# Kernel tuning notes

Hardware: AMD Instinct MI355X
Metric: run time of the kernel (lower is better)

The kernel has to match this reference:

```python
import jax, jax.numpy as jnp
import numpy as np

B, SEG, MEM, D, E, H = 4, 1024, 1024, 128, 128, 8  # model_dim == embed_dim required by module
TOTAL = SEG + MEM


def sinusoid_pos(length, e):
    # Transformer-XL relative sinusoid table, then flipped so row 0 = largest distance
    p = jnp.arange(length, dtype=jnp.float32)[:, None]
    j = jnp.arange(e, dtype=jnp.float32)[None, :]
    ang = p / jnp.power(jnp.float32(10000.0), 2.0 * j / e)
    enc = jnp.where((jnp.arange(e) % 2 == 0)[None, :], jnp.sin(ang), jnp.cos(ang))
    return enc[::-1]


def circulant_shift(b, shift):
    # b: (B, H, S, W). Row i of the index matrix is the rolled arange shifted by (shift - i).
    W = b.shape[-1]
    S = b.shape[-2]
    idx = jnp.roll(jnp.arange(W), shift)[::-1]
    idx2 = jnp.concatenate([idx, idx])
    win = idx2[jnp.arange(S)[:, None] + jnp.arange(W)[None, :]][:, ::-1]  # (S, W)
    return jnp.take_along_axis(b, win[None, None, :, :], axis=3)


def setup_inputs() -> dict:
    key = jax.random.key(0)
    ks = jax.random.split(key, 11)
    w = 0.02  # small init for linear weights (Linear default-ish scale)
    return {
        "x": jax.random.normal(ks[0], (B, SEG, D), dtype=jnp.float32),
        "mem": jax.random.normal(ks[1], (B, MEM, D), dtype=jnp.float32),
        "att_mask": jnp.zeros((SEG, TOTAL), dtype=bool),  # unused by the module's forward
        "u1": jax.random.normal(ks[2], (H, 1, E), dtype=jnp.float32),
        "u2": jax.random.normal(ks[3], (H, 1, E), dtype=jnp.float32),
        "w_q": jax.random.normal(ks[4], (D, H * E), dtype=jnp.float32) * w,
        "w_kv": jax.random.normal(ks[5], (D, 2 * H * E), dtype=jnp.float32) * w,
        "w_r": jax.random.normal(ks[6], (D, H * E), dtype=jnp.float32) * w,
        "w_mlp": jax.random.normal(ks[7], (H * E, D), dtype=jnp.float32) * w,
        "ln_g": jnp.ones((D,), dtype=jnp.float32),
        "ln_b": jnp.zeros((D,), dtype=jnp.float32),
    }


def reference(x, mem, att_mask, u1, u2, w_q, w_kv, w_r, w_mlp, ln_g, ln_b):
    bsz, seg, d = x.shape
    h = jnp.concatenate((mem, x), axis=1)          # (B, total, D)
    total = h.shape[1]
    mem_len = total - seg

    # NB: the original uses .view without transpose -> plain row-major reshape
    q = (x @ w_q).reshape(bsz, -1, seg, d)          # (B, H, S, E)
    kv = (h @ w_kv).reshape(2 * bsz, -1, total, d)  # (2B, H, T, E)
    k, v = kv[:bsz], kv[bsz:]

    pos = sinusoid_pos(total, d)                    # buffer pos[-total:]
    r = (pos @ w_r).reshape(-1, total, d)           # (H, T, E)

    b = jnp.einsum('bhse,hte->bhst', q, r)
    b = circulant_shift(b, -seg + 1)

    qk = jnp.einsum('bhse,bhte->bhst', q, k)
    u1k = jnp.einsum('he,bhte->bht', u1[:, 0], k)[:, :, None, :]
    u2r = jnp.einsum('he,hte->ht', u2[:, 0], r)[None, :, None, :]

    score = qk + b + u1k + u2r                      # (B, H, S, T)
    tri = (jnp.arange(total)[None, :] - jnp.arange(seg)[:, None]) <= mem_len
    score = jnp.where(tri[None, None], score, 0.0) / jnp.sqrt(jnp.float32(d))
    score = jnp.where(score == 0.0, -jnp.inf, score)  # faithful zeros->-inf trick
    score = jax.nn.softmax(score, axis=-1)

    att = jnp.einsum('bhst,bhte->bhse', score, v).reshape(bsz, seg, -1)
    y = att @ w_mlp + x
    mu = jnp.mean(y, axis=-1, keepdims=True)
    var = jnp.mean((y - mu) ** 2, axis=-1, keepdims=True)
    return (y - mu) / jnp.sqrt(var + 1e-5) * ln_g + ln_b
```

## Files before the change

### kernel.cpp

```cpp
#include <hip/hip_runtime.h>
#include <hip/hip_bf16.h>
#include <stdint.h>

typedef __bf16 bf16;
typedef __attribute__((ext_vector_type(8))) __bf16 bf16x8;
typedef __attribute__((ext_vector_type(4))) __bf16 bf16x4;
typedef __attribute__((ext_vector_type(4))) float f32x4;

#define KSC 0.12764932952880681f

__device__ __forceinline__ f32x4 MFMA(bf16x8 a, bf16x8 b, f32x4 c) {
  return __builtin_amdgcn_mfma_f32_16x16x32_bf16(a, b, c, 0, 0, 0);
}

__device__ __forceinline__ void GLL16(const void* g, void* l) {
  __builtin_amdgcn_global_load_lds(
      (const __attribute__((address_space(1))) void*)g,
      (__attribute__((address_space(3))) void*)l, 16, 0, 0);
}

__device__ __forceinline__ bf16 tobf(float f) { return (bf16)f; }

__global__ __launch_bounds__(256) void k_prep(
    const float* __restrict__ x, const float* __restrict__ mm,
    const float* __restrict__ wq, const float* __restrict__ wkv,
    const float* __restrict__ wr, const float* __restrict__ wmlp,
    bf16* __restrict__ posb, bf16* __restrict__ wq_bt, bf16* __restrict__ wkv_bt,
    bf16* __restrict__ wr_bt, bf16* __restrict__ wmlp_bt,
    bf16* __restrict__ xb, bf16* __restrict__ memb)
{
  int id = blockIdx.x * 256 + threadIdx.x;
  if (id < 262144) {
    int t = id >> 7, j = id & 127;
    float p = (float)(2047 - t);
    float ang = p * exp2f(-(float)j * 0.20762050593046264f);
    float v = ((j & 1) == 0) ? sinf(ang) : cosf(ang);
    posb[id] = tobf(v);
    return;
  }
  id -= 262144;
  if (id < 131072) { int k = id >> 10, n = id & 1023; wq_bt[n * 128 + k] = tobf(wq[id]); return; }
  id -= 131072;
  if (id < 262144) { int k = id >> 11, n = id & 2047; wkv_bt[n * 128 + k] = tobf(wkv[id]); return; }
  id -= 262144;
  if (id < 131072) { int k = id >> 10, n = id & 1023; wr_bt[n * 128 + k] = tobf(wr[id]); return; }
  id -= 131072;
  if (id < 131072) { int k = id >> 7, n = id & 127; wmlp_bt[n * 1024 + k] = tobf(wmlp[id]); return; }
  id -= 131072;
  if (id < 131072) {
    f32x4 v = *(const f32x4*)(x + (size_t)id * 4);
    bf16x4 o; o[0]=tobf(v[0]); o[1]=tobf(v[1]); o[2]=tobf(v[2]); o[3]=tobf(v[3]);
    *(bf16x4*)(xb + (size_t)id * 4) = o;
    return;
  }
  id -= 131072;
  if (id < 131072) {
    f32x4 v = *(const f32x4*)(mm + (size_t)id * 4);
    bf16x4 o; o[0]=tobf(v[0]); o[1]=tobf(v[1]); o[2]=tobf(v[2]); o[3]=tobf(v[3]);
    *(bf16x4*)(memb + (size_t)id * 4) = o;
  }
}

template <int MODE>
__global__ __launch_bounds__(256, 2) void k_proj(
    const bf16* __restrict__ asrc, const bf16* __restrict__ asrc2,
    const bf16* __restrict__ wbt, bf16* __restrict__ out0, bf16* __restrict__ out1,
    const float* __restrict__ u1, const float* __restrict__ u2)
{
  __shared__ bf16 As[64 * 128];
  __shared__ bf16 Bs[128 * 128];
  const int m0 = blockIdx.x * 64;
  const int n0 = blockIdx.y * 128;
  const int tid = threadIdx.x;
  const int w = tid >> 6, lane = tid & 63, g = lane >> 4, c = lane & 15;

#pragma unroll
  for (int it = 0; it < 4; ++it) {
    int ch = w * 256 + it * 64 + lane;
    int row = ch >> 4, cc = ch & 15;
    int scc = cc ^ (row & 7);
    const bf16* src;
    if (MODE == 1) {
      int rg = m0 + row;
      int bb = rg >> 11, t = rg & 2047;
      src = (t < 1024) ? (asrc2 + (size_t)(bb * 1024 + t) * 128)
                       : (asrc + (size_t)(bb * 1024 + (t - 1024)) * 128);
    } else {
      src = asrc + (size_t)(m0 + row) * 128;
    }
    GLL16(src + scc * 8, (char*)As + (w * 256 + it * 64) * 16);
  }
#pragma unroll
  for (int it = 0; it < 8; ++it) {
    int ch = w * 512 + it * 64 + lane;
    int n = ch >> 4, cc = ch & 15;
    int scc = cc ^ (n & 7);
    GLL16(wbt + (size_t)(n0 + n) * 128 + scc * 8, (char*)Bs + (w * 512 + it * 64) * 16);
  }
  __syncthreads();

  f32x4 acc[8] = {};
#pragma unroll
  for (int kk = 0; kk < 4; ++kk) {
    bf16x8 a = *(const bf16x8*)((const char*)As + (16 * w + c) * 256 + (((4 * kk + g) ^ (c & 7)) << 4));
#pragma unroll
    for (int fo = 0; fo < 8; ++fo) {
      bf16x8 b = *(const bf16x8*)((const char*)Bs + (16 * fo + c) * 256 + (((4 * kk + g) ^ (c & 7)) << 4));
      acc[fo] = MFMA(a, b, acc[fo]);
    }
  }

#pragma unroll
  for (int fo = 0; fo < 8; ++fo) {
#pragma unroll
    for (int j = 0; j < 4; ++j) {
      int rg = m0 + 16 * w + 4 * g + j;
      int cg = n0 + 16 * fo + c;
      float av = acc[fo][j];
      if (MODE == 0) {
        int b = rg >> 10, s2 = rg & 1023;
        int nn = s2 >> 7;
        int s = ((s2 & 127) << 3) | (cg >> 7);
        int e = cg & 127;
        size_t idx = ((size_t)((b * 8 + nn) * 1024 + s)) * 128 + e;
        out0[idx] = tobf((av + u1[nn * 128 + e]) * KSC);
        out1[idx] = tobf((av + u2[nn * 128 + e]) * KSC);
      } else if (MODE == 1) {
        int bb = rg >> 11, t = rg & 2047;
        int nn = (t >> 7) & 7;
        int hlf = (t >> 10) & 1;
        int t2 = ((t & 127) << 4) | (cg >> 7);
        int e = cg & 127;
        bf16 v = tobf(av);
        if (bb < 2)
          out0[((size_t)(((2 * bb + hlf) * 8 + nn) * 2048 + t2)) * 128 + e] = v;
        else
          out1[((size_t)(((2 * (bb - 2) + hlf) * 8 + nn) * 2048 + t2)) * 128 + e] = v;
      } else {
        int nn = rg >> 8;
        int t = ((rg & 255) << 3) | (cg >> 7);
        int e = cg & 127;
        bf16 v = tobf(av);
        out0[((size_t)(nn * 2112 + t)) * 128 + e] = v;
        if (t < 64) out0[((size_t)(nn * 2112 + 2048 + t)) * 128 + e] = v;
      }
    }
  }
}

__global__ __launch_bounds__(256) void k_vtrans(const bf16* __restrict__ vh, bf16* __restrict__ vht)
{
  __shared__ bf16 T[64][72];
  int bt = blockIdx.x * 64, be = blockIdx.y * 64, bh = blockIdx.z;
  const bf16* src = vh + (size_t)bh * 2048 * 128;
  bf16* dst = vht + (size_t)bh * 128 * 2048;
#pragma unroll
  for (int i2 = 0; i2 < 2; ++i2) {
    int ch = i2 * 256 + threadIdx.x;
    int tt = ch >> 3, cc = ch & 7;
    bf16x8 v = *(const bf16x8*)(src + (size_t)(bt + tt) * 128 + be + cc * 8);
    *(bf16x8*)&T[tt][cc * 8] = v;
  }
  __syncthreads();
#pragma unroll
  for (int i2 = 0; i2 < 2; ++i2) {
    int ch = i2 * 256 + threadIdx.x;
    int ee = ch >> 3, c2 = ch & 7;
    bf16x8 o;
#pragma unroll
    for (int m = 0; m < 8; ++m) o[m] = T[c2 * 8 + m][ee];
    *(bf16x8*)(dst + (size_t)(be + ee) * 2048 + bt + c2 * 8) = o;
  }
}

__global__ __launch_bounds__(256, 2) void k_flash(
    const bf16* __restrict__ qhk, const bf16* __restrict__ qhr,
    const bf16* __restrict__ kh, const bf16* __restrict__ vht,
    const bf16* __restrict__ rhe, bf16* __restrict__ att2)
{
  __shared__ bf16 Ks[2][64 * 128];
  __shared__ bf16 Vs[2][64 * 128];
  __shared__ char QRS[4][2688];

  const int x = blockIdx.x;
  const int bh = x & 31;
  const int qb = (x < 256) ? (x >> 5) : (15 - ((x - 256) >> 5));
  const int ib = bh >> 3, nh = bh & 7;
  const int s0 = qb * 64;
  const int tid = threadIdx.x;
  const int w = tid >> 6, lane = tid & 63, g = lane >> 4, c = lane & 15;

  const bf16* qkb  = qhk + (size_t)bh * 1024 * 128;
  const bf16* qrb  = qhr + (size_t)bh * 1024 * 128;
  const bf16* kbase = kh + (size_t)bh * 2048 * 128;
  const bf16* vbase = vht + (size_t)bh * 128 * 2048;
  const bf16* rbase = rhe + (size_t)nh * 2112 * 128;

  const int nt = qb + 17;

  const bf16 *kp0, *kp1, *vp0, *vp1, *vp2, *vp3;
  {
    int ch0 = w * 256 + lane;
    int ch1 = ch0 + 64;
    int r0 = ch0 >> 4, cc0 = ch0 & 15;
    int r1 = ch1 >> 4, cc1 = ch1 & 15;
    kp0 = kbase + (size_t)r0 * 128 + (cc0 ^ (r0 & 7)) * 8;
    kp1 = kbase + (size_t)r1 * 128 + (cc1 ^ (r1 & 7)) * 8;
    int e0 = ch0 >> 3, t0c = ch0 & 7;
    int e1 = ch1 >> 3, t1c = ch1 & 7;
    int e2 = e0 + 16, e3 = e1 + 16;
    vp0 = vbase + (size_t)e0 * 2048 + (t0c ^ (e0 & 7)) * 8;
    vp1 = vbase + (size_t)e1 * 2048 + (t1c ^ (e1 & 7)) * 8;
    vp2 = vbase + (size_t)e2 * 2048 + (t0c ^ (e2 & 7)) * 8;
    vp3 = vbase + (size_t)e3 * 2048 + (t1c ^ (e3 & 7)) * 8;
  }
  const int dof = (w * 256 + lane) * 16;

  auto stage = [&](char* Kd, char* Vd) {
    GLL16(kp0, Kd + dof);
    GLL16(kp1, Kd + dof + 1024);
    GLL16(kp0 + 1024, Kd + dof + 2048);
    GLL16(kp1 + 1024, Kd + dof + 3072);
    GLL16(vp0, Vd + dof);
    GLL16(vp1, Vd + dof + 1024);
    GLL16(vp2, Vd + dof + 2048);
    GLL16(vp3, Vd + dof + 3072);
    kp0 += 8192; kp1 += 8192;
    vp0 += 64; vp1 += 64; vp2 += 64; vp3 += 64;
  };

  bf16x8 qfK[4], qfR[4];
  {
    int srow = s0 + 16 * w + c;
#pragma unroll
    for (int kk = 0; kk < 4; ++kk) {
      qfK[kk] = *(const bf16x8*)(qkb + (size_t)srow * 128 + kk * 32 + g * 8);
      qfR[kk] = *(const bf16x8*)(qrb + (size_t)srow * 128 + kk * 32 + g * 8);
    }
  }

  bf16x8 rf[5][4];
  const bf16* rp[5];
  {
    const int L0 = 1008 - s0 - 16 * w + c;
#pragma unroll
    for (int f2 = 0; f2 < 5; ++f2) {
      rp[f2] = rbase + (size_t)(L0 + 16 * f2) * 128 + g * 8;
#pragma unroll
      for (int kk = 0; kk < 4; ++kk) rf[f2][kk] = *(const bf16x8*)(rp[f2] + kk * 32);
      rp[f2] += 64 * 128;
    }
  }

  f32x4 Ot[8] = {};
  float m_r = -1e30f, l_r = 0.f;

  stage((char*)Ks[0], (char*)Vs[0]);

  for (int tt = 0; tt < nt; ++tt) {
    __syncthreads();
    const bool notlast = (tt + 1 < nt);
    if (notlast) stage((char*)Ks[(tt + 1) & 1], (char*)Vs[(tt + 1) & 1]);

    const bf16* Kc = Ks[tt & 1];
    const bf16* Vc = Vs[tt & 1];

    f32x4 sacc[4] = {};
    __builtin_amdgcn_s_setprio(1);
#pragma unroll
    for (int kk = 0; kk < 4; ++kk) {
#pragma unroll
      for (int f = 0; f < 4; ++f) {
        bf16x8 kf = *(const bf16x8*)((const char*)Kc + (16 * f + c) * 256 + (((4 * kk + g) ^ (c & 7)) << 4));
        sacc[f] = MFMA(kf, qfK[kk], sacc[f]);
      }
    }
    f32x4 bacc[5] = {};
#pragma unroll
    for (int f2 = 0; f2 < 5; ++f2)
#pragma unroll
      for (int kk = 0; kk < 4; ++kk)
        bacc[f2] = MFMA(rf[f2][kk], qfR[kk], bacc[f2]);
    __builtin_amdgcn_s_setprio(0);

    bf16* qrw = (bf16*)QRS[w];
#pragma unroll
    for (int f2 = 0; f2 < 5; ++f2)
#pragma unroll
      for (int j = 0; j < 4; ++j)
        qrw[c * 82 + 16 * f2 + 4 * g + j] = tobf(bacc[f2][j]);

    if (notlast) {
#pragma unroll
      for (int f2 = 0; f2 < 5; ++f2) {
#pragma unroll
        for (int kk = 0; kk < 4; ++kk) rf[f2][kk] = *(const bf16x8*)(rp[f2] + kk * 32);
        rp[f2] += 64 * 128;
      }
    }

    float zv[4][4];
#pragma unroll
    for (int f = 0; f < 4; ++f)
#pragma unroll
      for (int j = 0; j < 4; ++j) {
        int tl = 16 * f + 4 * g + j;
        float z = sacc[f][j] + (float)qrw[c * 82 + (tl - c + 15)];
        if (!notlast && (tl > 16 * w + c)) z = -1e30f;
        zv[f][j] = z;
      }

    float pm = fmaxf(fmaxf(fmaxf(zv[0][0], zv[0][1]), fmaxf(zv[0][2], zv[0][3])),
                     fmaxf(fmaxf(zv[1][0], zv[1][1]), fmaxf(zv[1][2], zv[1][3])));
    float pm2 = fmaxf(fmaxf(fmaxf(zv[2][0], zv[2][1]), fmaxf(zv[2][2], zv[2][3])),
                      fmaxf(fmaxf(zv[3][0], zv[3][1]), fmaxf(zv[3][2], zv[3][3])));
    pm = fmaxf(pm, pm2);
    pm = fmaxf(pm, __shfl_xor(pm, 16));
    pm = fmaxf(pm, __shfl_xor(pm, 32));

    float alpha = 1.f;
    if (!__all(pm <= m_r + 8.0f)) {
      float mn = fmaxf(m_r, pm);
      alpha = exp2f(m_r - mn);
      m_r = mn;
      float at[4];
#pragma unroll
      for (int j = 0; j < 4; ++j) at[j] = __shfl(alpha, 20 * g + j);
#pragma unroll
      for (int fo = 0; fo < 8; ++fo)
#pragma unroll
        for (int j = 0; j < 4; ++j) Ot[fo][j] *= at[j];
    }

    float ps = 0.f;
#pragma unroll
    for (int f = 0; f < 4; ++f)
#pragma unroll
      for (int j = 0; j < 4; ++j) { float pp = exp2f(zv[f][j] - m_r); zv[f][j] = pp; ps += pp; }
    ps += __shfl_xor(ps, 16);
    ps += __shfl_xor(ps, 32);
    l_r = l_r * alpha + ps;

    bf16* pw = (bf16*)QRS[w];
#pragma unroll
    for (int f = 0; f < 4; ++f)
#pragma unroll
      for (int j = 0; j < 4; ++j) {
        int t = 16 * f + 4 * g + j;
        pw[c * 80 + ((((t >> 3) ^ (c & 7)) << 3) | (t & 7))] = tobf(zv[f][j]);
      }

    __builtin_amdgcn_s_setprio(1);
#pragma unroll
    for (int kk2 = 0; kk2 < 2; ++kk2) {
      bf16x8 pa = *(const bf16x8*)(pw + c * 80 + (((4 * kk2 + g) ^ (c & 7)) << 3));
#pragma unroll
      for (int fo = 0; fo < 8; ++fo) {
        int e = 16 * fo + c;
        bf16x8 vf = *(const bf16x8*)((const char*)Vc + e * 128 + (((4 * kk2 + g) ^ (c & 7)) << 4));
        Ot[fo] = MFMA(pa, vf, Ot[fo]);
      }
    }
    __builtin_amdgcn_s_setprio(0);
  }

  float linv[4];
#pragma unroll
  for (int j = 0; j < 4; ++j) linv[j] = 1.f / __shfl(l_r, 20 * g + j);
  bf16* ob = att2 + (size_t)ib * 1024 * 1024;
#pragma unroll
  for (int j = 0; j < 4; ++j) {
    int sg = s0 + 16 * w + 4 * g + j;
    size_t rowb = (size_t)(nh * 128 + (sg >> 3)) * 1024 + ((sg & 7) << 7);
#pragma unroll
    for (int fo = 0; fo < 8; ++fo)
      ob[rowb + 16 * fo + c] = tobf(Ot[fo][j] * linv[j]);
  }
}

__global__ __launch_bounds__(256, 2) void k_mlp(
    const bf16* __restrict__ att2, const bf16* __restrict__ wmlp_bt,
    const float* __restrict__ x, const float* __restrict__ lng, const float* __restrict__ lnb,
    float* __restrict__ out)
{
  __shared__ bf16 As[64 * 128];
  __shared__ bf16 Bs[128 * 128];
  const int m0 = blockIdx.x * 64;
  const int tid = threadIdx.x;
  const int w = tid >> 6, lane = tid & 63, g = lane >> 4, c = lane & 15;

  f32x4 acc[8] = {};
  for (int ks = 0; ks < 8; ++ks) {
    int k0 = ks * 128;
    __syncthreads();
#pragma unroll
    for (int it = 0; it < 4; ++it) {
      int ch = w * 256 + it * 64 + lane;
      int row = ch >> 4, cc = ch & 15;
      GLL16(att2 + (size_t)(m0 + row) * 1024 + k0 + ((cc ^ (row & 7)) * 8),
            (char*)As + (w * 256 + it * 64) * 16);
    }
#pragma unroll
    for (int it = 0; it < 8; ++it) {
      int ch = w * 512 + it * 64 + lane;
      int n = ch >> 4, cc = ch & 15;
      GLL16(wmlp_bt + (size_t)n * 1024 + k0 + ((cc ^ (n & 7)) * 8),
            (char*)Bs + (w * 512 + it * 64) * 16);
    }
    __syncthreads();
#pragma unroll
    for (int kk = 0; kk < 4; ++kk) {
      bf16x8 a = *(const bf16x8*)((const char*)As + (16 * w + c) * 256 + (((4 * kk + g) ^ (c & 7)) << 4));
#pragma unroll
      for (int fo = 0; fo < 8; ++fo) {
        bf16x8 b = *(const bf16x8*)((const char*)Bs + (16 * fo + c) * 256 + (((4 * kk + g) ^ (c & 7)) << 4));
        acc[fo] = MFMA(a, b, acc[fo]);
      }
    }
  }
#pragma unroll
  for (int j = 0; j < 4; ++j) {
    int rg = m0 + 16 * w + 4 * g + j;
    float y[8];
    float s1 = 0.f, s2 = 0.f;
#pragma unroll
    for (int fo = 0; fo < 8; ++fo) {
      float v = acc[fo][j] + x[(size_t)rg * 128 + 16 * fo + c];
      y[fo] = v; s1 += v; s2 += v * v;
    }
#pragma unroll
    for (int d = 1; d < 16; d <<= 1) { s1 += __shfl_xor(s1, d); s2 += __shfl_xor(s2, d); }
    float mu = s1 * 0.0078125f;
    float var = s2 * 0.0078125f - mu * mu;
    float rs = rsqrtf(var + 1e-5f);
#pragma unroll
    for (int fo = 0; fo < 8; ++fo) {
      int e = 16 * fo + c;
      out[(size_t)rg * 128 + e] = (y[fo] - mu) * rs * lng[e] + lnb[e];
    }
  }
}

extern "C" void kernel_launch(void* const* d_in, const int* in_sizes, int n_in,
                              void* d_out, int out_size, void* d_ws, size_t ws_size,
                              hipStream_t stream)
{
  const float* x    = (const float*)d_in[0];
  const float* mm   = (const float*)d_in[1];
  const float* u1   = (const float*)d_in[3];
  const float* u2   = (const float*)d_in[4];
  const float* wq   = (const float*)d_in[5];
  const float* wkv  = (const float*)d_in[6];
  const float* wr   = (const float*)d_in[7];
  const float* wmlp = (const float*)d_in[8];
  const float* lng  = (const float*)d_in[9];
  const float* lnb  = (const float*)d_in[10];
  float* out = (float*)d_out;

  char* p = (char*)d_ws;
  bf16* posb    = (bf16*)p;  p += (size_t)262144 * 2;
  bf16* wq_bt   = (bf16*)p;  p += (size_t)131072 * 2;
  bf16* wkv_bt  = (bf16*)p;  p += (size_t)262144 * 2;
  bf16* wr_bt   = (bf16*)p;  p += (size_t)131072 * 2;
  bf16* wmlp_bt = (bf16*)p;  p += (size_t)131072 * 2;
  bf16* xb      = (bf16*)p;  p += (size_t)524288 * 2;
  bf16* memb    = (bf16*)p;  p += (size_t)524288 * 2;
  bf16* qhk     = (bf16*)p;  p += (size_t)4 * 8 * 1024 * 128 * 2;
  bf16* qhr     = (bf16*)p;  p += (size_t)4 * 8 * 1024 * 128 * 2;
  bf16* kh      = (bf16*)p;  p += (size_t)4 * 8 * 2048 * 128 * 2;
  bf16* vh      = (bf16*)p;  p += (size_t)4 * 8 * 2048 * 128 * 2;
  bf16* vht     = (bf16*)p;  p += (size_t)4 * 8 * 2048 * 128 * 2;
  bf16* rhe     = (bf16*)p;  p += (size_t)8 * 2112 * 128 * 2;
  bf16* att2    = (bf16*)p;  p += (size_t)4 * 1024 * 1024 * 2;

  k_prep<<<dim3(4608), dim3(256), 0, stream>>>(x, mm, wq, wkv, wr, wmlp,
                                               posb, wq_bt, wkv_bt, wr_bt, wmlp_bt, xb, memb);
  k_proj<0><<<dim3(64, 8),   dim3(256), 0, stream>>>(xb,  (const bf16*)nullptr, wq_bt,  qhk, qhr, u1, u2);
  k_proj<1><<<dim3(128, 16), dim3(256), 0, stream>>>(xb,  memb,                 wkv_bt, kh,  vh,  nullptr, nullptr);
  k_proj<2><<<dim3(32, 8),   dim3(256), 0, stream>>>(posb,(const bf16*)nullptr, wr_bt,  rhe, (bf16*)nullptr, nullptr, nullptr);
  k_vtrans<<<dim3(32, 2, 32), dim3(256), 0, stream>>>(vh, vht);
  k_flash<<<dim3(512), dim3(256), 0, stream>>>(qhk, qhr, kh, vht, rhe, att2);
  k_mlp<<<dim3(64), dim3(256), 0, stream>>>(att2, wmlp_bt, x, lng, lnb, out);
}
```

Before: 273.9 us.

## Split flash attention over KV halves with combine kernel, single-buffer LDS

Splits each query block's key range into two halves processed by separate workgroups (1024 blocks instead of 512), writing fp16 partial outputs plus running max and sum, which a new combine kernel merges into att2. LDS drops to single-buffered K/V with staged loads interleaved around an extra barrier, allowing three blocks per CU. The prep kernel now transposes weights through shared-memory tiles for coalesced access and uses fast sin/cos intrinsics. This adds a combine pass and extra global traffic for the partials, and reduces load/compute overlap inside each block.

```diff
diff --git a/kernel.cpp b/kernel.cpp
--- a/kernel.cpp
+++ b/kernel.cpp
@@ -3,8 +3,10 @@
 #include <stdint.h>
 
 typedef __bf16 bf16;
+typedef _Float16 f16;
 typedef __attribute__((ext_vector_type(8))) __bf16 bf16x8;
 typedef __attribute__((ext_vector_type(4))) __bf16 bf16x4;
+typedef __attribute__((ext_vector_type(8))) _Float16 f16x8;
 typedef __attribute__((ext_vector_type(4))) float f32x4;
 
 #define KSC 0.12764932952880681f
@@ -29,35 +31,48 @@
     bf16* __restrict__ wr_bt, bf16* __restrict__ wmlp_bt,
     bf16* __restrict__ xb, bf16* __restrict__ memb)
 {
-  int id = blockIdx.x * 256 + threadIdx.x;
-  if (id < 262144) {
+  __shared__ float T[32][33];
+  const int b = blockIdx.x;
+  const int tid = threadIdx.x;
+  if (b < 1024) {
+    int id = b * 256 + tid;
     int t = id >> 7, j = id & 127;
     float p = (float)(2047 - t);
     float ang = p * exp2f(-(float)j * 0.20762050593046264f);
-    float v = ((j & 1) == 0) ? sinf(ang) : cosf(ang);
+    float v = ((j & 1) == 0) ? __sinf(ang) : __cosf(ang);
     posb[id] = tobf(v);
     return;
   }
-  id -= 262144;
-  if (id < 131072) { int k = id >> 10, n = id & 1023; wq_bt[n * 128 + k] = tobf(wq[id]); return; }
-  id -= 131072;
-  if (id < 262144) { int k = id >> 11, n = id & 2047; wkv_bt[n * 128 + k] = tobf(wkv[id]); return; }
-  id -= 262144;
-  if (id < 131072) { int k = id >> 10, n = id & 1023; wr_bt[n * 128 + k] = tobf(wr[id]); return; }
-  id -= 131072;
-  if (id < 131072) { int k = id >> 7, n = id & 127; wmlp_bt[n * 1024 + k] = tobf(wmlp[id]); return; }
-  id -= 131072;
-  if (id < 131072) {
-    f32x4 v = *(const f32x4*)(x + (size_t)id * 4);
-    bf16x4 o; o[0]=tobf(v[0]); o[1]=tobf(v[1]); o[2]=tobf(v[2]); o[3]=tobf(v[3]);
-    *(bf16x4*)(xb + (size_t)id * 4) = o;
+  if (b < 1664) {
+    int tb = b - 1024;
+    const float* src; bf16* dst; int R, C, r0, c0;
+    if (tb < 128)      { src = wq;   dst = wq_bt;   R = 128;  C = 1024; r0 = (tb >> 5) * 32;        c0 = (tb & 31) * 32; }
+    else if (tb < 384) { int t2 = tb - 128; src = wkv;  dst = wkv_bt;  R = 128;  C = 2048; r0 = (t2 >> 6) * 32; c0 = (t2 & 63) * 32; }
+    else if (tb < 512) { int t2 = tb - 384; src = wr;   dst = wr_bt;   R = 128;  C = 1024; r0 = (t2 >> 5) * 32; c0 = (t2 & 31) * 32; }
+    else               { int t2 = tb - 512; src = wmlp; dst = wmlp_bt; R = 1024; C = 128;  r0 = (t2 >> 2) * 32; c0 = (t2 & 3) * 32; }
+    int r = tid >> 3, c4 = (tid & 7) * 4;
+    f32x4 v = *(const f32x4*)(src + (size_t)(r0 + r) * C + c0 + c4);
+    T[r][c4] = v[0]; T[r][c4 + 1] = v[1]; T[r][c4 + 2] = v[2]; T[r][c4 + 3] = v[3];
+    __syncthreads();
+    bf16x4 o;
+#pragma unroll
+    for (int k = 0; k < 4; ++k) o[k] = tobf(T[c4 + k][r]);
+    *(bf16x4*)(dst + (size_t)(c0 + r) * R + r0 + c4) = o;
     return;
   }
-  id -= 131072;
-  if (id < 131072) {
-    f32x4 v = *(const f32x4*)(mm + (size_t)id * 4);
-    bf16x4 o; o[0]=tobf(v[0]); o[1]=tobf(v[1]); o[2]=tobf(v[2]); o[3]=tobf(v[3]);
-    *(bf16x4*)(memb + (size_t)id * 4) = o;
+  {
+    int cb = b - 1664;
+    if (cb < 512) {
+      int i = cb * 256 + tid;
+      f32x4 v = *(const f32x4*)(x + (size_t)i * 4);
+      bf16x4 o; o[0]=tobf(v[0]); o[1]=tobf(v[1]); o[2]=tobf(v[2]); o[3]=tobf(v[3]);
+      *(bf16x4*)(xb + (size_t)i * 4) = o;
+    } else {
+      int i = (cb - 512) * 256 + tid;
+      f32x4 v = *(const f32x4*)(mm + (size_t)i * 4);
+      bf16x4 o; o[0]=tobf(v[0]); o[1]=tobf(v[1]); o[2]=tobf(v[2]); o[3]=tobf(v[3]);
+      *(bf16x4*)(memb + (size_t)i * 4) = o;
+    }
   }
 }
 
@@ -173,30 +188,36 @@
   }
 }
 
-__global__ __launch_bounds__(256, 2) void k_flash(
+__global__ __launch_bounds__(256, 3) void k_flash(
     const bf16* __restrict__ qhk, const bf16* __restrict__ qhr,
     const bf16* __restrict__ kh, const bf16* __restrict__ vht,
-    const bf16* __restrict__ rhe, bf16* __restrict__ att2)
-{
-  __shared__ bf16 Ks[2][64 * 128];
-  __shared__ bf16 Vs[2][64 * 128];
+    const bf16* __restrict__ rhe,
+    f16* __restrict__ part_O, float* __restrict__ part_m, float* __restrict__ part_l)
+{
+  __shared__ bf16 Ks[64 * 128];
+  __shared__ bf16 Vs[64 * 128];
   __shared__ char QRS[4][2688];
 
   const int x = blockIdx.x;
-  const int bh = x & 31;
-  const int qb = (x < 256) ? (x >> 5) : (15 - ((x - 256) >> 5));
-  const int ib = bh >> 3, nh = bh & 7;
+  const int bh = x >> 5;
+  const int qb = (x >> 1) & 15;
+  const int half = x & 1;
+  const int pidx = x;
+  const int nh = bh & 7;
   const int s0 = qb * 64;
   const int tid = threadIdx.x;
   const int w = tid >> 6, lane = tid & 63, g = lane >> 4, c = lane & 15;
+
+  const int nt = qb + 17;
+  const int h = nt >> 1;
+  const int T0 = half ? h : 0;
+  const int Tend = half ? nt : h;
 
   const bf16* qkb  = qhk + (size_t)bh * 1024 * 128;
   const bf16* qrb  = qhr + (size_t)bh * 1024 * 128;
   const bf16* kbase = kh + (size_t)bh * 2048 * 128;
   const bf16* vbase = vht + (size_t)bh * 128 * 2048;
   const bf16* rbase = rhe + (size_t)nh * 2112 * 128;
-
-  const int nt = qb + 17;
 
   const bf16 *kp0, *kp1, *vp0, *vp1, *vp2, *vp3;
   {
@@ -204,28 +225,34 @@
     int ch1 = ch0 + 64;
     int r0 = ch0 >> 4, cc0 = ch0 & 15;
     int r1 = ch1 >> 4, cc1 = ch1 & 15;
-    kp0 = kbase + (size_t)r0 * 128 + (cc0 ^ (r0 & 7)) * 8;
-    kp1 = kbase + (size_t)r1 * 128 + (cc1 ^ (r1 & 7)) * 8;
+    size_t koff = (size_t)T0 * 64 * 128;
+    kp0 = kbase + koff + (size_t)r0 * 128 + (cc0 ^ (r0 & 7)) * 8;
+    kp1 = kbase + koff + (size_t)r1 * 128 + (cc1 ^ (r1 & 7)) * 8;
     int e0 = ch0 >> 3, t0c = ch0 & 7;
     int e1 = ch1 >> 3, t1c = ch1 & 7;
     int e2 = e0 + 16, e3 = e1 + 16;
-    vp0 = vbase + (size_t)e0 * 2048 + (t0c ^ (e0 & 7)) * 8;
-    vp1 = vbase + (size_t)e1 * 2048 + (t1c ^ (e1 & 7)) * 8;
-    vp2 = vbase + (size_t)e2 * 2048 + (t0c ^ (e2 & 7)) * 8;
-    vp3 = vbase + (size_t)e3 * 2048 + (t1c ^ (e3 & 7)) * 8;
+    int voff = T0 * 64;
+    vp0 = vbase + (size_t)e0 * 2048 + voff + (t0c ^ (e0 & 7)) * 8;
+    vp1 = vbase + (size_t)e1 * 2048 + voff + (t1c ^ (e1 & 7)) * 8;
+    vp2 = vbase + (size_t)e2 * 2048 + voff + (t0c ^ (e2 & 7)) * 8;
+    vp3 = vbase + (size_t)e3 * 2048 + voff + (t1c ^ (e3 & 7)) * 8;
   }
   const int dof = (w * 256 + lane) * 16;
 
-  auto stage = [&](char* Kd, char* Vd) {
+  auto stageK = [&]() {
+    char* Kd = (char*)Ks;
     GLL16(kp0, Kd + dof);
     GLL16(kp1, Kd + dof + 1024);
     GLL16(kp0 + 1024, Kd + dof + 2048);
     GLL16(kp1 + 1024, Kd + dof + 3072);
+    kp0 += 8192; kp1 += 8192;
+  };
+  auto stageV = [&]() {
+    char* Vd = (char*)Vs;
     GLL16(vp0, Vd + dof);
     GLL16(vp1, Vd + dof + 1024);
     GLL16(vp2, Vd + dof + 2048);
     GLL16(vp3, Vd + dof + 3072);
-    kp0 += 8192; kp1 += 8192;
     vp0 += 64; vp1 += 64; vp2 += 64; vp3 += 64;
   };
 
@@ -242,7 +269,7 @@
   bf16x8 rf[5][4];
   const bf16* rp[5];
   {
-    const int L0 = 1008 - s0 - 16 * w + c;
+    const int L0 = 1008 - s0 - 16 * w + c + 64 * T0;
 #pragma unroll
     for (int f2 = 0; f2 < 5; ++f2) {
       rp[f2] = rbase + (size_t)(L0 + 16 * f2) * 128 + g * 8;
@@ -255,15 +282,11 @@
   f32x4 Ot[8] = {};
   float m_r = -1e30f, l_r = 0.f;
 
-  stage((char*)Ks[0], (char*)Vs[0]);
-
-  for (int tt = 0; tt < nt; ++tt) {
+  stageK();
+
+  for (int tt = T0; tt < Tend; ++tt) {
     __syncthreads();
-    const bool notlast = (tt + 1 < nt);
-    if (notlast) stage((char*)Ks[(tt + 1) & 1], (char*)Vs[(tt + 1) & 1]);
-
-    const bf16* Kc = Ks[tt & 1];
-    const bf16* Vc = Vs[tt & 1];
+    stageV();
 
     f32x4 sacc[4] = {};
     __builtin_amdgcn_s_setprio(1);
@@ -271,7 +294,7 @@
     for (int kk = 0; kk < 4; ++kk) {
 #pragma unroll
       for (int f = 0; f < 4; ++f) {
-        bf16x8 kf = *(const bf16x8*)((const char*)Kc + (16 * f + c) * 256 + (((4 * kk + g) ^ (c & 7)) << 4));
+        bf16x8 kf = *(const bf16x8*)((const char*)Ks + (16 * f + c) * 256 + (((4 * kk + g) ^ (c & 7)) << 4));
         sacc[f] = MFMA(kf, qfK[kk], sacc[f]);
       }
     }
@@ -290,15 +313,7 @@
       for (int j = 0; j < 4; ++j)
         qrw[c * 82 + 16 * f2 + 4 * g + j] = tobf(bacc[f2][j]);
 
-    if (notlast) {
-#pragma unroll
-      for (int f2 = 0; f2 < 5; ++f2) {
-#pragma unroll
-        for (int kk = 0; kk < 4; ++kk) rf[f2][kk] = *(const bf16x8*)(rp[f2] + kk * 32);
-        rp[f2] += 64 * 128;
-      }
-    }
-
+    const bool lastT = (tt == nt - 1);
     float zv[4][4];
 #pragma unroll
     for (int f = 0; f < 4; ++f)
@@ -306,7 +321,7 @@
       for (int j = 0; j < 4; ++j) {
         int tl = 16 * f + 4 * g + j;
         float z = sacc[f][j] + (float)qrw[c * 82 + (tl - c + 15)];
-        if (!notlast && (tl > 16 * w + c)) z = -1e30f;
+        if (lastT && (tl > 16 * w + c)) z = -1e30f;
         zv[f][j] = z;
       }
 
@@ -350,6 +365,18 @@
         pw[c * 80 + ((((t >> 3) ^ (c & 7)) << 3) | (t & 7))] = tobf(zv[f][j]);
       }
 
+    __syncthreads();
+    const bool more = (tt + 1 < Tend);
+    if (more) stageK();
+    if (more) {
+#pragma unroll
+      for (int f2 = 0; f2 < 5; ++f2) {
+#pragma unroll
+        for (int kk = 0; kk < 4; ++kk) rf[f2][kk] = *(const bf16x8*)(rp[f2] + kk * 32);
+        rp[f2] += 64 * 128;
+      }
+    }
+
     __builtin_amdgcn_s_setprio(1);
 #pragma unroll
     for (int kk2 = 0; kk2 < 2; ++kk2) {
@@ -357,24 +384,59 @@
 #pragma unroll
       for (int fo = 0; fo < 8; ++fo) {
         int e = 16 * fo + c;
-        bf16x8 vf = *(const bf16x8*)((const char*)Vc + e * 128 + (((4 * kk2 + g) ^ (c & 7)) << 4));
+        bf16x8 vf = *(const bf16x8*)((const char*)Vs + e * 128 + (((4 * kk2 + g) ^ (c & 7)) << 4));
         Ot[fo] = MFMA(pa, vf, Ot[fo]);
       }
     }
     __builtin_amdgcn_s_setprio(0);
   }
 
+  if (g == 0) {
+    part_m[pidx * 64 + 16 * w + c] = m_r;
+    part_l[pidx * 64 + 16 * w + c] = l_r;
+  }
   float linv[4];
 #pragma unroll
   for (int j = 0; j < 4; ++j) linv[j] = 1.f / __shfl(l_r, 20 * g + j);
-  bf16* ob = att2 + (size_t)ib * 1024 * 1024;
+  f16* po = part_O + (size_t)pidx * 8192;
 #pragma unroll
   for (int j = 0; j < 4; ++j) {
-    int sg = s0 + 16 * w + 4 * g + j;
-    size_t rowb = (size_t)(nh * 128 + (sg >> 3)) * 1024 + ((sg & 7) << 7);
+    int sl = 16 * w + 4 * g + j;
 #pragma unroll
     for (int fo = 0; fo < 8; ++fo)
-      ob[rowb + 16 * fo + c] = tobf(Ot[fo][j] * linv[j]);
+      po[sl * 128 + 16 * fo + c] = (f16)(Ot[fo][j] * linv[j]);
+  }
+}
+
+__global__ __launch_bounds__(256) void k_combine(
+    const f16* __restrict__ part_O, const float* __restrict__ part_m,
+    const float* __restrict__ part_l, bf16* __restrict__ att2)
+{
+  int ss = blockIdx.x;
+  int bh = ss >> 4, qb = ss & 15;
+  int p1 = (bh << 5) | (qb << 1), p2 = p1 | 1;
+  int r = threadIdx.x >> 2;
+  int e0 = (threadIdx.x & 3) * 32;
+  float m1 = part_m[p1 * 64 + r], m2 = part_m[p2 * 64 + r];
+  float l1 = part_l[p1 * 64 + r], l2 = part_l[p2 * 64 + r];
+  float m = fmaxf(m1, m2);
+  float a1 = exp2f(m1 - m) * l1, a2 = exp2f(m2 - m) * l2;
+  float inv = 1.f / (a1 + a2);
+  a1 *= inv; a2 *= inv;
+  int sg = qb * 64 + r;
+  int ib = bh >> 3, nh = bh & 7;
+  bf16* ob = att2 + (size_t)ib * 1024 * 1024
+           + ((size_t)(nh * 128 + (sg >> 3))) * 1024 + ((sg & 7) << 7);
+  const f16* o1 = part_O + ((size_t)p1 * 64 + r) * 128 + e0;
+  const f16* o2 = part_O + ((size_t)p2 * 64 + r) * 128 + e0;
+#pragma unroll
+  for (int i = 0; i < 32; i += 8) {
+    f16x8 v1 = *(const f16x8*)(o1 + i);
+    f16x8 v2 = *(const f16x8*)(o2 + i);
+    bf16x8 o;
+#pragma unroll
+    for (int k = 0; k < 8; ++k) o[k] = tobf(a1 * (float)v1[k] + a2 * (float)v2[k]);
+    *(bf16x8*)(ob + e0 + i) = o;
   }
 }
 
@@ -473,12 +535,17 @@
   bf16* rhe     = (bf16*)p;  p += (size_t)8 * 2112 * 128 * 2;
   bf16* att2    = (bf16*)p;  p += (size_t)4 * 1024 * 1024 * 2;
 
-  k_prep<<<dim3(4608), dim3(256), 0, stream>>>(x, mm, wq, wkv, wr, wmlp,
+  f16*   part_O = (f16*)vh;
+  float* part_m = (float*)posb;
+  float* part_l = (float*)posb + 65536;
+
+  k_prep<<<dim3(2688), dim3(256), 0, stream>>>(x, mm, wq, wkv, wr, wmlp,
                                                posb, wq_bt, wkv_bt, wr_bt, wmlp_bt, xb, memb);
   k_proj<0><<<dim3(64, 8),   dim3(256), 0, stream>>>(xb,  (const bf16*)nullptr, wq_bt,  qhk, qhr, u1, u2);
   k_proj<1><<<dim3(128, 16), dim3(256), 0, stream>>>(xb,  memb,                 wkv_bt, kh,  vh,  nullptr, nullptr);
   k_proj<2><<<dim3(32, 8),   dim3(256), 0, stream>>>(posb,(const bf16*)nullptr, wr_bt,  rhe, (bf16*)nullptr, nullptr, nullptr);
   k_vtrans<<<dim3(32, 2, 32), dim3(256), 0, stream>>>(vh, vht);
-  k_flash<<<dim3(512), dim3(256), 0, stream>>>(qhk, qhr, kh, vht, rhe, att2);
+  k_flash<<<dim3(1024), dim3(256), 0, stream>>>(qhk, qhr, kh, vht, rhe, part_O, part_m, part_l);
+  k_combine<<<dim3(512), dim3(256), 0, stream>>>(part_O, part_m, part_l, att2);
   k_mlp<<<dim3(64), dim3(256), 0, stream>>>(att2, wmlp_bt, x, lng, lnb, out);
 }
```

Result: slower. 568.7 us (+107.6%).

## Tile weight transposes through LDS, use fast sincos, remap flash blocks per XCD

Applied to the files above, without the earlier changes.

The weight transposes in k_prep now go through a 32x33 shared-memory tile, so both the global reads and the writes are coalesced and vectorised. The old version did scattered scalar stores. The positional sinusoid uses the __sinf/__cosf intrinsics, which can lose accuracy at large angles before bf16 rounding. The flash kernel block index is remapped so that blocks for the same batch-head land on the same XCD (x&7), improving K/V/R reuse in L2 while keeping the long/short q-block balancing. These are several independent changes across two kernels.

```diff
diff --git a/kernel.cpp b/kernel.cpp
--- a/kernel.cpp
+++ b/kernel.cpp
@@ -29,35 +29,48 @@
     bf16* __restrict__ wr_bt, bf16* __restrict__ wmlp_bt,
     bf16* __restrict__ xb, bf16* __restrict__ memb)
 {
-  int id = blockIdx.x * 256 + threadIdx.x;
-  if (id < 262144) {
+  __shared__ float T[32][33];
+  const int b = blockIdx.x;
+  const int tid = threadIdx.x;
+  if (b < 1024) {
+    int id = b * 256 + tid;
     int t = id >> 7, j = id & 127;
     float p = (float)(2047 - t);
     float ang = p * exp2f(-(float)j * 0.20762050593046264f);
-    float v = ((j & 1) == 0) ? sinf(ang) : cosf(ang);
+    float v = ((j & 1) == 0) ? __sinf(ang) : __cosf(ang);
     posb[id] = tobf(v);
     return;
   }
-  id -= 262144;
-  if (id < 131072) { int k = id >> 10, n = id & 1023; wq_bt[n * 128 + k] = tobf(wq[id]); return; }
-  id -= 131072;
-  if (id < 262144) { int k = id >> 11, n = id & 2047; wkv_bt[n * 128 + k] = tobf(wkv[id]); return; }
-  id -= 262144;
-  if (id < 131072) { int k = id >> 10, n = id & 1023; wr_bt[n * 128 + k] = tobf(wr[id]); return; }
-  id -= 131072;
-  if (id < 131072) { int k = id >> 7, n = id & 127; wmlp_bt[n * 1024 + k] = tobf(wmlp[id]); return; }
-  id -= 131072;
-  if (id < 131072) {
-    f32x4 v = *(const f32x4*)(x + (size_t)id * 4);
-    bf16x4 o; o[0]=tobf(v[0]); o[1]=tobf(v[1]); o[2]=tobf(v[2]); o[3]=tobf(v[3]);
-    *(bf16x4*)(xb + (size_t)id * 4) = o;
+  if (b < 1664) {
+    int tb = b - 1024;
+    const float* src; bf16* dst; int R, C, r0, c0;
+    if (tb < 128)      { src = wq;   dst = wq_bt;   R = 128;  C = 1024; r0 = (tb >> 5) * 32;        c0 = (tb & 31) * 32; }
+    else if (tb < 384) { int t2 = tb - 128; src = wkv;  dst = wkv_bt;  R = 128;  C = 2048; r0 = (t2 >> 6) * 32; c0 = (t2 & 63) * 32; }
+    else if (tb < 512) { int t2 = tb - 384; src = wr;   dst = wr_bt;   R = 128;  C = 1024; r0 = (t2 >> 5) * 32; c0 = (t2 & 31) * 32; }
+    else               { int t2 = tb - 512; src = wmlp; dst = wmlp_bt; R = 1024; C = 128;  r0 = (t2 >> 2) * 32; c0 = (t2 & 3) * 32; }
+    int r = tid >> 3, c4 = (tid & 7) * 4;
+    f32x4 v = *(const f32x4*)(src + (size_t)(r0 + r) * C + c0 + c4);
+    T[r][c4] = v[0]; T[r][c4 + 1] = v[1]; T[r][c4 + 2] = v[2]; T[r][c4 + 3] = v[3];
+    __syncthreads();
+    bf16x4 o;
+#pragma unroll
+    for (int k = 0; k < 4; ++k) o[k] = tobf(T[c4 + k][r]);
+    *(bf16x4*)(dst + (size_t)(c0 + r) * R + r0 + c4) = o;
     return;
   }
-  id -= 131072;
-  if (id < 131072) {
-    f32x4 v = *(const f32x4*)(mm + (size_t)id * 4);
-    bf16x4 o; o[0]=tobf(v[0]); o[1]=tobf(v[1]); o[2]=tobf(v[2]); o[3]=tobf(v[3]);
-    *(bf16x4*)(memb + (size_t)id * 4) = o;
+  {
+    int cb = b - 1664;
+    if (cb < 512) {
+      int i = cb * 256 + tid;
+      f32x4 v = *(const f32x4*)(x + (size_t)i * 4);
+      bf16x4 o; o[0]=tobf(v[0]); o[1]=tobf(v[1]); o[2]=tobf(v[2]); o[3]=tobf(v[3]);
+      *(bf16x4*)(xb + (size_t)i * 4) = o;
+    } else {
+      int i = (cb - 512) * 256 + tid;
+      f32x4 v = *(const f32x4*)(mm + (size_t)i * 4);
+      bf16x4 o; o[0]=tobf(v[0]); o[1]=tobf(v[1]); o[2]=tobf(v[2]); o[3]=tobf(v[3]);
+      *(bf16x4*)(memb + (size_t)i * 4) = o;
+    }
   }
 }
 
@@ -183,8 +196,10 @@
   __shared__ char QRS[4][2688];
 
   const int x = blockIdx.x;
-  const int bh = x & 31;
-  const int qb = (x < 256) ? (x >> 5) : (15 - ((x - 256) >> 5));
+  const int xcd = x & 7;
+  const int k2 = x >> 3;
+  const int bh = 8 * (k2 & 3) + xcd;
+  const int qb = (k2 < 32) ? (k2 >> 2) : (23 - (k2 >> 2));
   const int ib = bh >> 3, nh = bh & 7;
   const int s0 = qb * 64;
   const int tid = threadIdx.x;
@@ -216,7 +231,9 @@
   }
   const int dof = (w * 256 + lane) * 16;
 
-  auto stage = [&](char* Kd, char* Vd) {
+  auto stage = [&](int pb) {
+    char* Kd = (char*)Ks[pb];
+    char* Vd = (char*)Vs[pb];
     GLL16(kp0, Kd + dof);
     GLL16(kp1, Kd + dof + 1024);
     GLL16(kp0 + 1024, Kd + dof + 2048);
@@ -255,12 +272,12 @@
   f32x4 Ot[8] = {};
   float m_r = -1e30f, l_r = 0.f;
 
-  stage((char*)Ks[0], (char*)Vs[0]);
+  stage(0);
 
   for (int tt = 0; tt < nt; ++tt) {
     __syncthreads();
     const bool notlast = (tt + 1 < nt);
-    if (notlast) stage((char*)Ks[(tt + 1) & 1], (char*)Vs[(tt + 1) & 1]);
+    if (notlast) stage((tt + 1) & 1);
 
     const bf16* Kc = Ks[tt & 1];
     const bf16* Vc = Vs[tt & 1];
@@ -473,7 +490,7 @@
   bf16* rhe     = (bf16*)p;  p += (size_t)8 * 2112 * 128 * 2;
   bf16* att2    = (bf16*)p;  p += (size_t)4 * 1024 * 1024 * 2;
 
-  k_prep<<<dim3(4608), dim3(256), 0, stream>>>(x, mm, wq, wkv, wr, wmlp,
+  k_prep<<<dim3(2688), dim3(256), 0, stream>>>(x, mm, wq, wkv, wr, wmlp,
                                                posb, wq_bt, wkv_bt, wr_bt, wmlp_bt, xb, memb);
   k_proj<0><<<dim3(64, 8),   dim3(256), 0, stream>>>(xb,  (const bf16*)nullptr, wq_bt,  qhk, qhr, u1, u2);
   k_proj<1><<<dim3(128, 16), dim3(256), 0, stream>>>(xb,  memb,                 wkv_bt, kh,  vh,  nullptr, nullptr);
```

Result: no change. 269.9 us (-1.4%).
